# Performance work log

Hardware: AMD Instinct MI355X
Metric: run time of the kernel (lower is better)

Reference implementation:

```python
import jax, jax.numpy as jnp
import numpy as np
import math

D_MODEL = 1024
NUM_HEADS = 16
D_HEAD = D_MODEL // NUM_HEADS
BATCH = 2
SEQ = 2048
ROPE_BASE = 10000.0


def get_rotary_embedding(seq_len, d_head):
    # standard RoPE tables: cos/sin of shape [seq_len, d_head]
    inv_freq = 1.0 / (ROPE_BASE ** (jnp.arange(0, d_head, 2, dtype=jnp.float32) / d_head))
    t = jnp.arange(seq_len, dtype=jnp.float32)
    freqs = jnp.outer(t, inv_freq)                      # [S, d_head/2]
    emb = jnp.concatenate([freqs, freqs], axis=-1)      # [S, d_head]
    return jnp.cos(emb), jnp.sin(emb)


def rotate_half(x):
    x1, x2 = jnp.split(x, 2, axis=-1)
    return jnp.concatenate([-x2, x1], axis=-1)


def apply_rotary_pos_emb(x, cos, sin):
    # x: [B, H, S, Dh]; cos/sin: [S, Dh] broadcast over B, H
    return x * cos[None, None, :, :] + rotate_half(x) * sin[None, None, :, :]


def setup_inputs() -> dict:
    key = jax.random.key(0)
    ks = jax.random.split(key, 9)
    s = 1.0 / math.sqrt(D_MODEL)
    inp = {
        "x":  jax.random.normal(ks[0], (BATCH, SEQ, D_MODEL), dtype=jnp.float32),
        "Wq": jax.random.uniform(ks[1], (D_MODEL, D_MODEL), jnp.float32, -s, s),
        "bq": jnp.zeros((D_MODEL,), jnp.float32),
        "Wk": jax.random.uniform(ks[2], (D_MODEL, D_MODEL), jnp.float32, -s, s),
        "bk": jnp.zeros((D_MODEL,), jnp.float32),
        "Wv": jax.random.uniform(ks[3], (D_MODEL, D_MODEL), jnp.float32, -s, s),
        "bv": jnp.zeros((D_MODEL,), jnp.float32),
        "Wo": jax.random.uniform(ks[4], (D_MODEL, D_MODEL), jnp.float32, -s, s),
        "bo": jnp.zeros((D_MODEL,), jnp.float32),
    }
    return inp


def reference(x, Wq, bq, Wk, bk, Wv, bv, Wo, bo) -> jnp.ndarray:
    B, S, _ = x.shape
    H, Dh = NUM_HEADS, D_HEAD

    def proj(W, b):
        y = jnp.einsum('bsd,ed->bse', x, W) + b          # nn.Linear: x @ W^T + b
        return y.reshape(B, S, H, Dh).transpose(0, 2, 1, 3)  # [B,H,S,Dh]

    Q = proj(Wq, bq)
    K = proj(Wk, bk)
    V = proj(Wv, bv)

    cos, sin = get_rotary_embedding(S, Dh)
    Q = apply_rotary_pos_emb(Q, cos, sin)
    K = apply_rotary_pos_emb(K, cos, sin)

    scores = jnp.einsum('bhqd,bhkd->bhqk', Q, K) / math.sqrt(Dh)  # [B,H,S,S]
    causal = jnp.tril(jnp.ones((S, S), dtype=bool))
    scores = jnp.where(causal[None, None, :, :], scores, -jnp.inf)
    attn = jax.nn.softmax(scores, axis=-1)
    # dropout is identity in eval / p=0
    context = jnp.einsum('bhqk,bhkd->bhqd', attn, V)               # [B,H,S,Dh]
    context = context.transpose(0, 2, 1, 3).reshape(B, S, H * Dh)
    return jnp.einsum('bsd,ed->bse', context, Wo) + bo
```

## Files before the change

### kernel.cpp

```cpp
#include <hip/hip_runtime.h>
#include <hip/hip_bf16.h>
#include <math.h>

typedef __attribute__((ext_vector_type(8))) short short8;
typedef __attribute__((ext_vector_type(8))) __bf16 bf16x8;
typedef __attribute__((ext_vector_type(4))) float f32x4;
typedef __attribute__((ext_vector_type(16))) float f32x16;

#define D_MODEL 1024
#define NUM_HEADS 16
#define D_HEAD 64
#define BATCH 2
#define SEQ 2048
#define BH (BATCH * NUM_HEADS)
#define MTOT (BATCH * SEQ)

__device__ inline f32x4 mfma16(short8 a, short8 b, f32x4 c) {
  return __builtin_amdgcn_mfma_f32_16x16x32_bf16(
      __builtin_bit_cast(bf16x8, a), __builtin_bit_cast(bf16x8, b), c, 0, 0, 0);
}

__device__ inline f32x16 mfma32(short8 a, short8 b, f32x16 c) {
  return __builtin_amdgcn_mfma_f32_32x32x16_bf16(
      __builtin_bit_cast(bf16x8, a), __builtin_bit_cast(bf16x8, b), c, 0, 0, 0);
}

__device__ inline unsigned short f2b(float f) {
  __hip_bfloat16 h = __float2bfloat16(f);
  return __builtin_bit_cast(unsigned short, h);
}

__device__ inline unsigned cvt_pk_bf16(float lo, float hi) {
  unsigned r;
  asm("v_cvt_pk_bf16_f32 %0, %1, %2" : "=v"(r) : "v"(lo), "v"(hi));
  return r;
}

__device__ inline float exp2_hw(float x) {
  float r;
  asm("v_exp_f32 %0, %1" : "=v"(r) : "v"(x));
  return r;
}

__device__ inline void permlane32_swap(unsigned& a, unsigned& b) {
  asm("v_permlane32_swap_b32 %0, %1" : "+v"(a), "+v"(b));
}

__device__ __forceinline__ void wait_barrier_vm0() {
  asm volatile("s_waitcnt vmcnt(0)\n\ts_barrier" ::: "memory");
}

#define GLOAD_LDS16(gaddr, laddr)                                              \
  __builtin_amdgcn_global_load_lds(                                            \
      (const __attribute__((address_space(1))) void*)(gaddr),                  \
      (__attribute__((address_space(3))) void*)(laddr), 16, 0, 0)

__global__ void cvt_f32_bf16(const float* __restrict__ in,
                             unsigned short* __restrict__ out, int n) {
  int i = (blockIdx.x * 256 + threadIdx.x) * 4;
  if (i >= n) return;
  float4 v = *(const float4*)(in + i);
  ushort4 o;
  o.x = f2b(v.x); o.y = f2b(v.y); o.z = f2b(v.z); o.w = f2b(v.w);
  *(ushort4*)(out + i) = o;
}

__global__ void cvt4_f32_bf16(const float* __restrict__ w0, const float* __restrict__ w1,
                              const float* __restrict__ w2, const float* __restrict__ w3,
                              unsigned short* __restrict__ o0, unsigned short* __restrict__ o1,
                              unsigned short* __restrict__ o2, unsigned short* __restrict__ o3,
                              int n) {
  const float* in; unsigned short* out;
  switch (blockIdx.y) {
    case 0: in = w0; out = o0; break;
    case 1: in = w1; out = o1; break;
    case 2: in = w2; out = o2; break;
    default: in = w3; out = o3; break;
  }
  int i = (blockIdx.x * 256 + threadIdx.x) * 4;
  if (i >= n) return;
  float4 v = *(const float4*)(in + i);
  ushort4 o;
  o.x = f2b(v.x); o.y = f2b(v.y); o.z = f2b(v.z); o.w = f2b(v.w);
  *(ushort4*)(out + i) = o;
}

__global__ void trig_kernel(float2* __restrict__ tct) {
  int idx = blockIdx.x * 256 + threadIdx.x;
  int i = idx & 31;
  int s = idx >> 5;
  float inv = powf(10000.0f, -(float)i / 32.0f);
  float t = (float)s * inv;
  tct[idx] = make_float2(cosf(t), sinf(t));
}

#define STAGE64(t, bufi)                                                        \
  do {                                                                          \
    const int _k0 = (t) * 64;                                                   \
    const int _gc = ((lane & 7) ^ (lane >> 3)) * 8;                             \
    const int _lc = (lane & 7) * 8;                                             \
    for (int j = 0; j < 4; j++) {                                               \
      const int _r = w * 32 + j * 8 + (lane >> 3);                              \
      GLOAD_LDS16(&A[(size_t)(bm + _r) * D_MODEL + _k0 + _gc], &As[bufi][_r][_lc]); \
      GLOAD_LDS16(&Bp[(size_t)(bn + _r) * D_MODEL + _k0 + _gc], &Bs[bufi][_r][_lc]); \
    }                                                                           \
  } while (0)

#define KLOOP64()                                                               \
  do {                                                                          \
    const int NT = D_MODEL / 64;                                                \
    STAGE64(0, 0);                                                              \
    for (int t = 0; t < NT; ++t) {                                              \
      const int cur = t & 1;                                                    \
      wait_barrier_vm0();                                                       \
      if (t + 1 < NT) STAGE64(t + 1, cur ^ 1);                                  \
      for (int kk = 0; kk < 2; kk++) {                                          \
        short8 af[4], bf4[4];                                                   \
        for (int mi = 0; mi < 4; mi++)                                          \
          af[mi] = *(const short8*)&As[cur][wr + mi * 16 + fr]                  \
                                         [(kk * 32 + fk) ^ ((fr & 7) << 3)];    \
        for (int ni = 0; ni < 4; ni++)                                          \
          bf4[ni] = *(const short8*)&Bs[cur][wc + ni * 16 + fr]                 \
                                          [(kk * 32 + fk) ^ ((fr & 7) << 3)];   \
        __builtin_amdgcn_s_setprio(1);                                          \
        for (int mi = 0; mi < 4; mi++)                                          \
          for (int ni = 0; ni < 4; ni++)                                        \
            acc[mi][ni] = mfma16(af[mi], bf4[ni], acc[mi][ni]);                 \
        __builtin_amdgcn_s_setprio(0);                                          \
      }                                                                         \
    }                                                                           \
  } while (0)

__global__ __launch_bounds__(256) void gemm_qkv(
    const unsigned short* __restrict__ A,
    const unsigned short* __restrict__ Bp,
    const float* __restrict__ bq, const float* __restrict__ bk,
    const float* __restrict__ bv,
    const float2* __restrict__ tct,
    unsigned short* __restrict__ Qb, unsigned short* __restrict__ Kb,
    unsigned short* __restrict__ Vt) {
  __shared__ unsigned short As[2][128][64];
  __shared__ unsigned short Bs[2][128][64];
  const int bm = blockIdx.y * 128;
  const int bn = blockIdx.x * 128;
  const int tid = threadIdx.x;
  const int lane = tid & 63;
  const int w = tid >> 6;
  const int wr = (w >> 1) * 64, wc = (w & 1) * 64;
  const int fr = lane & 15;
  const int g = lane >> 4;
  const int fk = g * 8;

  f32x4 acc[4][4] = {};
  KLOOP64();

  const int type = bn >> 10;
  const int cloc = (bn & 1023) + wc;
  if (type <= 1) {
    const float* bias = (type == 0) ? bq : bk;
    unsigned short* outp = (type == 0) ? Qb : Kb;
    const float SC = (type == 0) ? 0.125f * 1.44269504f : 1.0f;
    const int h = cloc >> 6;
    for (int mi = 0; mi < 4; mi++)
      for (int r = 0; r < 4; r++) {
        int row = bm + wr + mi * 16 + g * 4 + r;
        int b = row >> 11, s = row & (SEQ - 1);
        size_t base = (((size_t)(b * NUM_HEADS + h)) * SEQ + s) * 64;
        for (int ni = 0; ni < 2; ni++) {
          int i = ni * 16 + fr;
          float x0 = acc[mi][ni][r] + bias[cloc + i];
          float x1 = acc[mi][ni + 2][r] + bias[cloc + i + 32];
          float2 cs = tct[s * 32 + i];
          outp[base + i]      = f2b((x0 * cs.x - x1 * cs.y) * SC);
          outp[base + i + 32] = f2b((x1 * cs.x + x0 * cs.y) * SC);
        }
      }
  } else {
    for (int mi = 0; mi < 4; mi++) {
      int row0 = bm + wr + mi * 16 + g * 4;
      int b = row0 >> 11, s0 = row0 & (SEQ - 1);
      for (int ni = 0; ni < 4; ni++) {
        int col = cloc + ni * 16 + fr;
        int h = col >> 6, dh = col & 63;
        float bvv = bv[col];
        uint2 pk = make_uint2(
            cvt_pk_bf16(acc[mi][ni][0] + bvv, acc[mi][ni][1] + bvv),
            cvt_pk_bf16(acc[mi][ni][2] + bvv, acc[mi][ni][3] + bvv));
        *(uint2*)&Vt[(((size_t)(b * NUM_HEADS + h)) * 64 + dh) * SEQ + s0] = pk;
      }
    }
  }
}

__global__ __launch_bounds__(256) void gemm_out(
    const unsigned short* __restrict__ A,
    const unsigned short* __restrict__ Bp,
    const float* __restrict__ bias,
    float* __restrict__ outf) {
  __shared__ unsigned short As[2][128][64];
  __shared__ unsigned short Bs[2][128][64];
  const int bm = blockIdx.y * 128;
  const int bn = blockIdx.x * 128;
  const int tid = threadIdx.x;
  const int lane = tid & 63;
  const int w = tid >> 6;
  const int wr = (w >> 1) * 64, wc = (w & 1) * 64;
  const int fr = lane & 15;
  const int g = lane >> 4;
  const int fk = g * 8;

  f32x4 acc[4][4] = {};
  KLOOP64();

  for (int mi = 0; mi < 4; mi++)
    for (int ni = 0; ni < 4; ni++)
      for (int r = 0; r < 4; r++) {
        int row = bm + wr + mi * 16 + g * 4 + r;
        int col = bn + wc + ni * 16 + fr;
        outf[(size_t)row * D_MODEL + col] = acc[mi][ni][r] + bias[col];
      }
}

__global__ __launch_bounds__(256) void flash_attn(
    const unsigned short* __restrict__ Q,
    const unsigned short* __restrict__ Km,
    const unsigned short* __restrict__ Vt,
    unsigned short* __restrict__ ctx) {
  __shared__ unsigned short Ks[64 * 64];
  __shared__ unsigned short Vs[64 * 64];
  const int bh = blockIdx.x;
  const int by = blockIdx.y;
  const int qt = (by < 8) ? (15 - by) : (by - 8);
  const int tid = threadIdx.x;
  const int lane = tid & 63;
  const int w = tid >> 6;
  const int q31 = lane & 31;
  const int hi = lane >> 5;

  const unsigned short* Qp = Q + (size_t)bh * SEQ * 64;
  const unsigned short* Kp = Km + (size_t)bh * SEQ * 64;
  const unsigned short* Vp = Vt + (size_t)bh * 64 * SEQ;
  const int b = bh >> 4, h = bh & 15;

  const int qbase = qt * 128;
  const int qrow0 = qbase + w * 32;
  const int wmax = qrow0 + 31;
  const int q = qrow0 + q31;

  short8 qf[4];
  for (int s = 0; s < 4; s++)
    qf[s] = *(const short8*)&Qp[(size_t)q * 64 + s * 16 + hi * 8];

  const int srow = tid >> 2;
  const int ss0 = (tid & 3) * 2, ss1 = ss0 + 1;
  const int lw0 = srow * 64 + ((ss0 ^ (srow & 7)) * 8);
  const int lw1 = srow * 64 + ((ss1 ^ (srow & 7)) * 8);

  short8 krA = *(const short8*)&Kp[(size_t)srow * 64 + ss0 * 8];
  short8 krB = *(const short8*)&Kp[(size_t)srow * 64 + ss1 * 8];
  short8 vrA = *(const short8*)&Vp[(size_t)srow * SEQ + ss0 * 8];
  short8 vrB = *(const short8*)&Vp[(size_t)srow * SEQ + ss1 * 8];

  f32x16 oacc0 = {}, oacc1 = {};
  float lq = 0.f;
  const int NSTEPS = 2 * qt + 2;

  for (int step = 0; step < NSTEPS; ++step) {
    const int kbase = step * 64;
    *(short8*)&Ks[lw0] = krA;
    *(short8*)&Ks[lw1] = krB;
    *(short8*)&Vs[lw0] = vrA;
    *(short8*)&Vs[lw1] = vrB;
    __syncthreads();
    if (step + 1 < NSTEPS) {
      const int nk = kbase + 64;
      krA = *(const short8*)&Kp[(size_t)(nk + srow) * 64 + ss0 * 8];
      krB = *(const short8*)&Kp[(size_t)(nk + srow) * 64 + ss1 * 8];
      vrA = *(const short8*)&Vp[(size_t)srow * SEQ + nk + ss0 * 8];
      vrB = *(const short8*)&Vp[(size_t)srow * SEQ + nk + ss1 * 8];
    }

    if (kbase <= wmax) {
      for (int kt = 0; kt < 2; kt++) {
        const int ktb = kbase + kt * 32;
        if (ktb <= wmax) {
          f32x16 sacc = {};
          const int krow = kt * 32 + q31;
          const int kro = krow * 64;
          const int ksw = krow & 7;
          for (int s = 0; s < 4; s++) {
            short8 kf = *(const short8*)&Ks[kro + (((s * 2 + hi) ^ ksw) * 8)];
            sacc = mfma32(kf, qf[s], sacc);
          }
          const bool maskT = (ktb + 31 > qrow0);
          float p[16];
          float rs = 0.f;
#pragma unroll
          for (int reg = 0; reg < 16; reg++) {
            float sv = sacc[reg];
            if (maskT) {
              int key = ktb + (reg & 3) + 8 * (reg >> 2) + 4 * hi;
              sv = (key <= q) ? sv : -INFINITY;
            }
            p[reg] = exp2_hw(sv);
            rs += p[reg];
          }
          lq += rs;
          short8 paf[2];
#pragma unroll
          for (int sl = 0; sl < 2; sl++) {
            const int o = sl * 8;
            unsigned a0 = cvt_pk_bf16(p[o + 0], p[o + 1]);
            unsigned b0 = cvt_pk_bf16(p[o + 4], p[o + 5]);
            permlane32_swap(a0, b0);
            unsigned a1 = cvt_pk_bf16(p[o + 2], p[o + 3]);
            unsigned b1 = cvt_pk_bf16(p[o + 6], p[o + 7]);
            permlane32_swap(a1, b1);
            uint4 u = make_uint4(a0, a1, b0, b1);
            paf[sl] = __builtin_bit_cast(short8, u);
          }
#pragma unroll
          for (int dt = 0; dt < 2; dt++) {
            const int vrow = dt * 32 + q31;
            const int vro = vrow * 64;
            const int vsw = vrow & 7;
#pragma unroll
            for (int sl = 0; sl < 2; sl++) {
              short8 vf = *(const short8*)&Vs[vro + (((kt * 4 + sl * 2 + hi) ^ vsw) * 8)];
              if (dt == 0) oacc0 = mfma32(paf[sl], vf, oacc0);
              else         oacc1 = mfma32(paf[sl], vf, oacc1);
            }
          }
        }
      }
    }
    __syncthreads();
  }

  lq += __shfl_xor(lq, 32);
#pragma unroll
  for (int reg = 0; reg < 16; reg++) {
    const int crow = (reg & 3) + 8 * (reg >> 2) + 4 * hi;
    const float linv = 1.f / __shfl(lq, crow);
    const int row = qrow0 + crow;
    size_t base = ((size_t)b * SEQ + row) * D_MODEL + h * 64 + q31;
    ctx[base]      = f2b(oacc0[reg] * linv);
    ctx[base + 32] = f2b(oacc1[reg] * linv);
  }
}

extern "C" void kernel_launch(void* const* d_in, const int* in_sizes, int n_in,
                              void* d_out, int out_size, void* d_ws, size_t ws_size,
                              hipStream_t stream) {
  const float* x  = (const float*)d_in[0];
  const float* Wq = (const float*)d_in[1];
  const float* bq = (const float*)d_in[2];
  const float* Wk = (const float*)d_in[3];
  const float* bk = (const float*)d_in[4];
  const float* Wv = (const float*)d_in[5];
  const float* bv = (const float*)d_in[6];
  const float* Wo = (const float*)d_in[7];
  const float* bo = (const float*)d_in[8];
  float* out = (float*)d_out;

  char* ws = (char*)d_ws;
  size_t off = 0;
  auto alloc = [&](size_t bytes) {
    char* p = ws + off;
    off += (bytes + 255) & ~(size_t)255;
    return p;
  };
  unsigned short* xb   = (unsigned short*)alloc((size_t)MTOT * D_MODEL * 2);
  unsigned short* wqkv = (unsigned short*)alloc((size_t)3 * D_MODEL * D_MODEL * 2);
  unsigned short* wob  = (unsigned short*)alloc((size_t)D_MODEL * D_MODEL * 2);
  unsigned short* Qb   = (unsigned short*)alloc((size_t)BH * SEQ * 64 * 2);
  unsigned short* Kb   = (unsigned short*)alloc((size_t)BH * SEQ * 64 * 2);
  unsigned short* Vt   = (unsigned short*)alloc((size_t)BH * 64 * SEQ * 2);
  unsigned short* ctxb = (unsigned short*)alloc((size_t)MTOT * D_MODEL * 2);
  float2* tct = (float2*)alloc((size_t)SEQ * 32 * 8);

  int nx = MTOT * D_MODEL;
  int nw = D_MODEL * D_MODEL;
  cvt_f32_bf16<<<nx / 1024, 256, 0, stream>>>(x, xb, nx);
  cvt4_f32_bf16<<<dim3(nw / 1024, 4), 256, 0, stream>>>(
      Wq, Wk, Wv, Wo, wqkv, wqkv + nw, wqkv + 2 * (size_t)nw, wob, nw);
  trig_kernel<<<SEQ * 32 / 256, 256, 0, stream>>>(tct);

  gemm_qkv<<<dim3(3 * D_MODEL / 128, MTOT / 128), 256, 0, stream>>>(
      xb, wqkv, bq, bk, bv, tct, Qb, Kb, Vt);

  flash_attn<<<dim3(BH, 16), 256, 0, stream>>>(Qb, Kb, Vt, ctxb);

  gemm_out<<<dim3(D_MODEL / 128, MTOT / 128), 256, 0, stream>>>(ctxb, wob, bo, out);
}
```

Measured before the change: 123.9 us.

## Shrink flash attention blocks to 64 query rows with two waves, longest-first order

The flash attention kernel now uses 128-thread blocks covering 64 query rows instead of 256-thread blocks covering 128, doubling the grid to 32 query tiles per head. Tiles are scheduled heaviest-first (descending qb) instead of the previous paired ordering. Each thread now stages four K and four V vectors per step. The smaller blocks cut wasted causal work at the diagonal and give finer load balance. The cost is that each K/V tile loaded into shared memory is reused by half as many query rows.

```diff
diff --git a/kernel.cpp b/kernel.cpp
--- a/kernel.cpp
+++ b/kernel.cpp
@@ -221,7 +221,7 @@
       }
 }
 
-__global__ __launch_bounds__(256) void flash_attn(
+__global__ __launch_bounds__(128) void flash_attn(
     const unsigned short* __restrict__ Q,
     const unsigned short* __restrict__ Km,
     const unsigned short* __restrict__ Vt,
@@ -229,8 +229,7 @@
   __shared__ unsigned short Ks[64 * 64];
   __shared__ unsigned short Vs[64 * 64];
   const int bh = blockIdx.x;
-  const int by = blockIdx.y;
-  const int qt = (by < 8) ? (15 - by) : (by - 8);
+  const int qb = 31 - (int)blockIdx.y;
   const int tid = threadIdx.x;
   const int lane = tid & 63;
   const int w = tid >> 6;
@@ -242,94 +241,96 @@
   const unsigned short* Vp = Vt + (size_t)bh * 64 * SEQ;
   const int b = bh >> 4, h = bh & 15;
 
-  const int qbase = qt * 128;
-  const int qrow0 = qbase + w * 32;
+  const int qrow0 = qb * 64 + w * 32;
   const int wmax = qrow0 + 31;
   const int q = qrow0 + q31;
 
   short8 qf[4];
+#pragma unroll
   for (int s = 0; s < 4; s++)
     qf[s] = *(const short8*)&Qp[(size_t)q * 64 + s * 16 + hi * 8];
 
-  const int srow = tid >> 2;
-  const int ss0 = (tid & 3) * 2, ss1 = ss0 + 1;
-  const int lw0 = srow * 64 + ((ss0 ^ (srow & 7)) * 8);
-  const int lw1 = srow * 64 + ((ss1 ^ (srow & 7)) * 8);
-
-  short8 krA = *(const short8*)&Kp[(size_t)srow * 64 + ss0 * 8];
-  short8 krB = *(const short8*)&Kp[(size_t)srow * 64 + ss1 * 8];
-  short8 vrA = *(const short8*)&Vp[(size_t)srow * SEQ + ss0 * 8];
-  short8 vrB = *(const short8*)&Vp[(size_t)srow * SEQ + ss1 * 8];
+  const int srow = tid >> 1;
+  const int sb = (tid & 1) * 4;
+  short8 kst[4], vst[4];
+#pragma unroll
+  for (int j = 0; j < 4; j++) {
+    kst[j] = *(const short8*)&Kp[(size_t)srow * 64 + (sb + j) * 8];
+    vst[j] = *(const short8*)&Vp[(size_t)srow * SEQ + (sb + j) * 8];
+  }
 
   f32x16 oacc0 = {}, oacc1 = {};
   float lq = 0.f;
-  const int NSTEPS = 2 * qt + 2;
+  const int NSTEPS = qb + 1;
 
   for (int step = 0; step < NSTEPS; ++step) {
     const int kbase = step * 64;
-    *(short8*)&Ks[lw0] = krA;
-    *(short8*)&Ks[lw1] = krB;
-    *(short8*)&Vs[lw0] = vrA;
-    *(short8*)&Vs[lw1] = vrB;
+#pragma unroll
+    for (int j = 0; j < 4; j++) {
+      const int off = srow * 64 + (((sb + j) ^ (srow & 7)) * 8);
+      *(short8*)&Ks[off] = kst[j];
+      *(short8*)&Vs[off] = vst[j];
+    }
     __syncthreads();
     if (step + 1 < NSTEPS) {
       const int nk = kbase + 64;
-      krA = *(const short8*)&Kp[(size_t)(nk + srow) * 64 + ss0 * 8];
-      krB = *(const short8*)&Kp[(size_t)(nk + srow) * 64 + ss1 * 8];
-      vrA = *(const short8*)&Vp[(size_t)srow * SEQ + nk + ss0 * 8];
-      vrB = *(const short8*)&Vp[(size_t)srow * SEQ + nk + ss1 * 8];
+#pragma unroll
+      for (int j = 0; j < 4; j++) {
+        kst[j] = *(const short8*)&Kp[(size_t)(nk + srow) * 64 + (sb + j) * 8];
+        vst[j] = *(const short8*)&Vp[(size_t)srow * SEQ + nk + (sb + j) * 8];
+      }
     }
 
-    if (kbase <= wmax) {
-      for (int kt = 0; kt < 2; kt++) {
-        const int ktb = kbase + kt * 32;
-        if (ktb <= wmax) {
-          f32x16 sacc = {};
-          const int krow = kt * 32 + q31;
-          const int kro = krow * 64;
-          const int ksw = krow & 7;
-          for (int s = 0; s < 4; s++) {
-            short8 kf = *(const short8*)&Ks[kro + (((s * 2 + hi) ^ ksw) * 8)];
-            sacc = mfma32(kf, qf[s], sacc);
+#pragma unroll
+    for (int kt = 0; kt < 2; kt++) {
+      const int ktb = kbase + kt * 32;
+      if (ktb <= wmax) {
+        f32x16 sacc = {};
+        const int krow = kt * 32 + q31;
+        const int kro = krow * 64;
+        const int ksw = krow & 7;
+#pragma unroll
+        for (int s = 0; s < 4; s++) {
+          short8 kf = *(const short8*)&Ks[kro + (((s * 2 + hi) ^ ksw) * 8)];
+          sacc = mfma32(kf, qf[s], sacc);
+        }
+        const bool maskT = (ktb + 31 > qrow0);
+        float p[16];
+        float rs = 0.f;
+#pragma unroll
+        for (int reg = 0; reg < 16; reg++) {
+          float sv = sacc[reg];
+          if (maskT) {
+            int key = ktb + (reg & 3) + 8 * (reg >> 2) + 4 * hi;
+            sv = (key <= q) ? sv : -INFINITY;
           }
-          const bool maskT = (ktb + 31 > qrow0);
-          float p[16];
-          float rs = 0.f;
-#pragma unroll
-          for (int reg = 0; reg < 16; reg++) {
-            float sv = sacc[reg];
-            if (maskT) {
-              int key = ktb + (reg & 3) + 8 * (reg >> 2) + 4 * hi;
-              sv = (key <= q) ? sv : -INFINITY;
-            }
-            p[reg] = exp2_hw(sv);
-            rs += p[reg];
-          }
-          lq += rs;
-          short8 paf[2];
+          p[reg] = exp2_hw(sv);
+          rs += p[reg];
+        }
+        lq += rs;
+        short8 paf[2];
+#pragma unroll
+        for (int sl = 0; sl < 2; sl++) {
+          const int o = sl * 8;
+          unsigned a0 = cvt_pk_bf16(p[o + 0], p[o + 1]);
+          unsigned b0 = cvt_pk_bf16(p[o + 4], p[o + 5]);
+          permlane32_swap(a0, b0);
+          unsigned a1 = cvt_pk_bf16(p[o + 2], p[o + 3]);
+          unsigned b1 = cvt_pk_bf16(p[o + 6], p[o + 7]);
+          permlane32_swap(a1, b1);
+          uint4 u = make_uint4(a0, a1, b0, b1);
+          paf[sl] = __builtin_bit_cast(short8, u);
+        }
+#pragma unroll
+        for (int dt = 0; dt < 2; dt++) {
+          const int vrow = dt * 32 + q31;
+          const int vro = vrow * 64;
+          const int vsw = vrow & 7;
 #pragma unroll
           for (int sl = 0; sl < 2; sl++) {
-            const int o = sl * 8;
-            unsigned a0 = cvt_pk_bf16(p[o + 0], p[o + 1]);
-            unsigned b0 = cvt_pk_bf16(p[o + 4], p[o + 5]);
-            permlane32_swap(a0, b0);
-            unsigned a1 = cvt_pk_bf16(p[o + 2], p[o + 3]);
-            unsigned b1 = cvt_pk_bf16(p[o + 6], p[o + 7]);
-            permlane32_swap(a1, b1);
-            uint4 u = make_uint4(a0, a1, b0, b1);
-            paf[sl] = __builtin_bit_cast(short8, u);
-          }
-#pragma unroll
-          for (int dt = 0; dt < 2; dt++) {
-            const int vrow = dt * 32 + q31;
-            const int vro = vrow * 64;
-            const int vsw = vrow & 7;
-#pragma unroll
-            for (int sl = 0; sl < 2; sl++) {
-              short8 vf = *(const short8*)&Vs[vro + (((kt * 4 + sl * 2 + hi) ^ vsw) * 8)];
-              if (dt == 0) oacc0 = mfma32(paf[sl], vf, oacc0);
-              else         oacc1 = mfma32(paf[sl], vf, oacc1);
-            }
+            short8 vf = *(const short8*)&Vs[vro + (((kt * 4 + sl * 2 + hi) ^ vsw) * 8)];
+            if (dt == 0) oacc0 = mfma32(paf[sl], vf, oacc0);
+            else         oacc1 = mfma32(paf[sl], vf, oacc1);
           }
         }
       }
@@ -389,7 +390,7 @@
   gemm_qkv<<<dim3(3 * D_MODEL / 128, MTOT / 128), 256, 0, stream>>>(
       xb, wqkv, bq, bk, bv, tct, Qb, Kb, Vt);
 
-  flash_attn<<<dim3(BH, 16), 256, 0, stream>>>(Qb, Kb, Vt, ctxb);
+  flash_attn<<<dim3(BH, 32), 128, 0, stream>>>(Qb, Kb, Vt, ctxb);
 
   gemm_out<<<dim3(D_MODEL / 128, MTOT / 128), 256, 0, stream>>>(ctxb, wob, bo, out);
 }
```

After: 127.9 us. 1.03x slower.

## Split long causal query tiles across KV chunks with separate combine kernel

Applied to the files above, without the earlier changes.

Flash attention now splits each query tile's key range into chunks of up to 8 KV steps, so long tiles are spread across up to four blocks (split-K / flash-decoding style). Partial unnormalized outputs and row sums go to fp32 workspace, and a new combine kernel sums them and normalizes. This works without max rescaling because the original kernel already uses a fixed-offset exp. The aim is to balance the causal workload and raise the grid from 512 to 1280 blocks. The cost is extra fp32 partial-output traffic and one more kernel launch.

```diff
diff --git a/kernel.cpp b/kernel.cpp
--- a/kernel.cpp
+++ b/kernel.cpp
@@ -225,12 +225,23 @@
     const unsigned short* __restrict__ Q,
     const unsigned short* __restrict__ Km,
     const unsigned short* __restrict__ Vt,
-    unsigned short* __restrict__ ctx) {
+    unsigned short* __restrict__ ctx,
+    float* __restrict__ Opart,
+    float* __restrict__ Lpart) {
   __shared__ unsigned short Ks[64 * 64];
   __shared__ unsigned short Vs[64 * 64];
-  const int bh = blockIdx.x;
-  const int by = blockIdx.y;
-  const int qt = (by < 8) ? (15 - by) : (by - 8);
+  const int x = blockIdx.x;
+  const int bh = blockIdx.y;
+  int qt, ci;
+  if (x < 4)       { qt = x;                  ci = 0; }
+  else if (x < 12) { qt = 4 + ((x - 4) >> 1); ci = (x - 4) & 1; }
+  else if (x < 24) { qt = 8 + (x - 12) / 3;   ci = (x - 12) % 3; }
+  else             { qt = 12 + ((x - 24) >> 2); ci = (x - 24) & 3; }
+  const int T = 2 * qt + 2;
+  const int step0 = ci * 8;
+  const int stepEnd = min(step0 + 8, T);
+  const bool multi = (qt >= 4);
+
   const int tid = threadIdx.x;
   const int lane = tid & 63;
   const int w = tid >> 6;
@@ -248,6 +259,7 @@
   const int q = qrow0 + q31;
 
   short8 qf[4];
+#pragma unroll
   for (int s = 0; s < 4; s++)
     qf[s] = *(const short8*)&Qp[(size_t)q * 64 + s * 16 + hi * 8];
 
@@ -256,23 +268,23 @@
   const int lw0 = srow * 64 + ((ss0 ^ (srow & 7)) * 8);
   const int lw1 = srow * 64 + ((ss1 ^ (srow & 7)) * 8);
 
-  short8 krA = *(const short8*)&Kp[(size_t)srow * 64 + ss0 * 8];
-  short8 krB = *(const short8*)&Kp[(size_t)srow * 64 + ss1 * 8];
-  short8 vrA = *(const short8*)&Vp[(size_t)srow * SEQ + ss0 * 8];
-  short8 vrB = *(const short8*)&Vp[(size_t)srow * SEQ + ss1 * 8];
+  const int kv0 = step0 * 64;
+  short8 krA = *(const short8*)&Kp[(size_t)(kv0 + srow) * 64 + ss0 * 8];
+  short8 krB = *(const short8*)&Kp[(size_t)(kv0 + srow) * 64 + ss1 * 8];
+  short8 vrA = *(const short8*)&Vp[(size_t)srow * SEQ + kv0 + ss0 * 8];
+  short8 vrB = *(const short8*)&Vp[(size_t)srow * SEQ + kv0 + ss1 * 8];
 
   f32x16 oacc0 = {}, oacc1 = {};
   float lq = 0.f;
-  const int NSTEPS = 2 * qt + 2;
-
-  for (int step = 0; step < NSTEPS; ++step) {
+
+  for (int step = step0; step < stepEnd; ++step) {
     const int kbase = step * 64;
     *(short8*)&Ks[lw0] = krA;
     *(short8*)&Ks[lw1] = krB;
     *(short8*)&Vs[lw0] = vrA;
     *(short8*)&Vs[lw1] = vrB;
     __syncthreads();
-    if (step + 1 < NSTEPS) {
+    if (step + 1 < stepEnd) {
       const int nk = kbase + 64;
       krA = *(const short8*)&Kp[(size_t)(nk + srow) * 64 + ss0 * 8];
       krB = *(const short8*)&Kp[(size_t)(nk + srow) * 64 + ss1 * 8];
@@ -281,6 +293,7 @@
     }
 
     if (kbase <= wmax) {
+#pragma unroll
       for (int kt = 0; kt < 2; kt++) {
         const int ktb = kbase + kt * 32;
         if (ktb <= wmax) {
@@ -288,6 +301,7 @@
           const int krow = kt * 32 + q31;
           const int kro = krow * 64;
           const int ksw = krow & 7;
+#pragma unroll
           for (int s = 0; s < 4; s++) {
             short8 kf = *(const short8*)&Ks[kro + (((s * 2 + hi) ^ ksw) * 8)];
             sacc = mfma32(kf, qf[s], sacc);
@@ -338,14 +352,61 @@
   }
 
   lq += __shfl_xor(lq, 32);
-#pragma unroll
-  for (int reg = 0; reg < 16; reg++) {
-    const int crow = (reg & 3) + 8 * (reg >> 2) + 4 * hi;
-    const float linv = 1.f / __shfl(lq, crow);
-    const int row = qrow0 + crow;
-    size_t base = ((size_t)b * SEQ + row) * D_MODEL + h * 64 + q31;
-    ctx[base]      = f2b(oacc0[reg] * linv);
-    ctx[base + 32] = f2b(oacc1[reg] * linv);
+
+  if (!multi) {
+#pragma unroll
+    for (int reg = 0; reg < 16; reg++) {
+      const int crow = (reg & 3) + 8 * (reg >> 2) + 4 * hi;
+      const float linv = 1.f / __shfl(lq, crow);
+      const int row = qrow0 + crow;
+      size_t base = ((size_t)b * SEQ + row) * D_MODEL + h * 64 + q31;
+      ctx[base]      = f2b(oacc0[reg] * linv);
+      ctx[base + 32] = f2b(oacc1[reg] * linv);
+    }
+  } else {
+    const size_t cbase = (((size_t)bh * 12 + (qt - 4)) * 4 + ci);
+    if (hi == 0) Lpart[cbase * 128 + w * 32 + q31] = lq;
+#pragma unroll
+    for (int reg = 0; reg < 16; reg++) {
+      const int crow = (reg & 3) + 8 * (reg >> 2) + 4 * hi;
+      const int r = w * 32 + crow;
+      float* Op = &Opart[(cbase * 128 + r) * 64 + q31];
+      Op[0]  = oacc0[reg];
+      Op[32] = oacc1[reg];
+    }
+  }
+}
+
+__global__ __launch_bounds__(256) void combine(
+    const float* __restrict__ Opart, const float* __restrict__ Lpart,
+    unsigned short* __restrict__ ctx) {
+  const int qtp = blockIdx.x;
+  const int bh = blockIdx.y;
+  const int qt = qtp + 4;
+  const int nc = (2 * qt + 9) >> 3;
+  const int b = bh >> 4, h = bh & 15;
+  const int t = threadIdx.x;
+  for (int it = 0; it < 4; ++it) {
+    const int e = it * 2048 + t * 8;
+    const int r = e >> 6, dh = e & 63;
+    float acc[8] = {};
+    float ls = 0.f;
+    for (int ci = 0; ci < nc; ++ci) {
+      const size_t base = (((size_t)bh * 12 + qtp) * 4 + ci) * 128 + r;
+      const float* Op = Opart + base * 64 + dh;
+      float4 a = *(const float4*)Op;
+      float4 c = *(const float4*)(Op + 4);
+      acc[0] += a.x; acc[1] += a.y; acc[2] += a.z; acc[3] += a.w;
+      acc[4] += c.x; acc[5] += c.y; acc[6] += c.z; acc[7] += c.w;
+      ls += Lpart[base];
+    }
+    const float inv = 1.f / ls;
+    unsigned short o[8];
+#pragma unroll
+    for (int j = 0; j < 8; j++) o[j] = f2b(acc[j] * inv);
+    const int row = qt * 128 + r;
+    *(short8*)&ctx[((size_t)b * SEQ + row) * D_MODEL + h * 64 + dh] =
+        *(short8*)o;
   }
 }
 
@@ -378,6 +439,8 @@
   unsigned short* Vt   = (unsigned short*)alloc((size_t)BH * 64 * SEQ * 2);
   unsigned short* ctxb = (unsigned short*)alloc((size_t)MTOT * D_MODEL * 2);
   float2* tct = (float2*)alloc((size_t)SEQ * 32 * 8);
+  float* Opart = (float*)alloc((size_t)32 * 12 * 4 * 128 * 64 * 4);
+  float* Lpart = (float*)alloc((size_t)32 * 12 * 4 * 128 * 4);
 
   int nx = MTOT * D_MODEL;
   int nw = D_MODEL * D_MODEL;
@@ -389,7 +452,8 @@
   gemm_qkv<<<dim3(3 * D_MODEL / 128, MTOT / 128), 256, 0, stream>>>(
       xb, wqkv, bq, bk, bv, tct, Qb, Kb, Vt);
 
-  flash_attn<<<dim3(BH, 16), 256, 0, stream>>>(Qb, Kb, Vt, ctxb);
+  flash_attn<<<dim3(40, BH), 256, 0, stream>>>(Qb, Kb, Vt, ctxb, Opart, Lpart);
+  combine<<<dim3(12, BH), 256, 0, stream>>>(Opart, Lpart, ctxb);
 
   gemm_out<<<dim3(D_MODEL / 128, MTOT / 128), 256, 0, stream>>>(ctxb, wob, bo, out);
 }
```

Measured after the change: 130.1 us. 1.05x slower.

## Use 256x256 tiles with 4-stage pipelined loads in QKV GEMM

Applied to the files above, without the earlier changes.

Rewrites the QKV projection GEMM to use 256x256 output tiles with 512 threads (8 waves, each computing 128x64). The K step drops to 32, and LDS is split into a 4-buffer ring filled three stages ahead, with partial vmcnt waits. The goal is more operand reuse per byte loaded and better latency hiding. The grid shrinks to 12x16=192 blocks, which may underfill the 256 CUs, and register pressure from 32 accumulators per lane rises.

```diff
diff --git a/kernel.cpp b/kernel.cpp
--- a/kernel.cpp
+++ b/kernel.cpp
@@ -48,6 +48,12 @@
 
 __device__ __forceinline__ void wait_barrier_vm0() {
   asm volatile("s_waitcnt vmcnt(0)\n\ts_barrier" ::: "memory");
+}
+__device__ __forceinline__ void wait_barrier_vm4() {
+  asm volatile("s_waitcnt vmcnt(4)\n\ts_barrier" ::: "memory");
+}
+__device__ __forceinline__ void wait_barrier_vm8() {
+  asm volatile("s_waitcnt vmcnt(8)\n\ts_barrier" ::: "memory");
 }
 
 #define GLOAD_LDS16(gaddr, laddr)                                              \
@@ -92,6 +98,109 @@
   float inv = powf(10000.0f, -(float)i / 32.0f);
   float t = (float)s * inv;
   tct[idx] = make_float2(cosf(t), sinf(t));
+}
+
+__global__ __launch_bounds__(512) void gemm_qkv(
+    const unsigned short* __restrict__ A,
+    const unsigned short* __restrict__ Bp,
+    const float* __restrict__ bq, const float* __restrict__ bk,
+    const float* __restrict__ bv,
+    const float2* __restrict__ tct,
+    unsigned short* __restrict__ Qb, unsigned short* __restrict__ Kb,
+    unsigned short* __restrict__ Vt) {
+  __shared__ unsigned short As[4][256][32];
+  __shared__ unsigned short Bs[4][256][32];
+  const int bm = blockIdx.y * 256;
+  const int bn = blockIdx.x * 256;
+  const int tid = threadIdx.x;
+  const int lane = tid & 63;
+  const int wid = tid >> 6;
+  const int wr = (wid >> 2) * 128;
+  const int wc = (wid & 3) * 64;
+  const int fr = lane & 15;
+  const int g = lane >> 4;
+  const int fk = g * 8;
+  const int rsw = (fr & 3) << 3;
+
+  int srow0 = tid >> 2,               slc0 = (tid & 3) * 8;
+  int srow1 = (512 + tid) >> 2,       slc1 = ((512 + tid) & 3) * 8;
+  int sgc0 = (((tid & 3) ^ (srow0 & 3)) * 8);
+  int sgc1 = ((((512 + tid) & 3) ^ (srow1 & 3)) * 8);
+
+#define QSTAGE(t, bi)                                                          \
+  do {                                                                         \
+    const int _k0 = (t) * 32;                                                  \
+    GLOAD_LDS16(&A[(size_t)(bm + srow0) * D_MODEL + _k0 + sgc0], &As[bi][srow0][slc0]); \
+    GLOAD_LDS16(&Bp[(size_t)(bn + srow0) * D_MODEL + _k0 + sgc0], &Bs[bi][srow0][slc0]); \
+    GLOAD_LDS16(&A[(size_t)(bm + srow1) * D_MODEL + _k0 + sgc1], &As[bi][srow1][slc1]); \
+    GLOAD_LDS16(&Bp[(size_t)(bn + srow1) * D_MODEL + _k0 + sgc1], &Bs[bi][srow1][slc1]); \
+  } while (0)
+
+  f32x4 acc[8][4] = {};
+  const int NT = D_MODEL / 32;
+
+  QSTAGE(0, 0);
+  QSTAGE(1, 1);
+  QSTAGE(2, 2);
+  for (int t = 0; t < NT; ++t) {
+    if (t + 2 < NT)      wait_barrier_vm8();
+    else if (t + 1 < NT) wait_barrier_vm4();
+    else                 wait_barrier_vm0();
+    if (t + 3 < NT) QSTAGE(t + 3, (t + 3) & 3);
+    const int cur = t & 3;
+    short8 af[8], bf4[4];
+#pragma unroll
+    for (int mi = 0; mi < 8; mi++)
+      af[mi] = *(const short8*)&As[cur][wr + mi * 16 + fr][fk ^ rsw];
+#pragma unroll
+    for (int ni = 0; ni < 4; ni++)
+      bf4[ni] = *(const short8*)&Bs[cur][wc + ni * 16 + fr][fk ^ rsw];
+    __builtin_amdgcn_s_setprio(1);
+#pragma unroll
+    for (int mi = 0; mi < 8; mi++)
+#pragma unroll
+      for (int ni = 0; ni < 4; ni++)
+        acc[mi][ni] = mfma16(af[mi], bf4[ni], acc[mi][ni]);
+    __builtin_amdgcn_s_setprio(0);
+  }
+
+  const int type = bn >> 10;
+  const int cloc = (bn & 1023) + wc;
+  if (type <= 1) {
+    const float* bias = (type == 0) ? bq : bk;
+    unsigned short* outp = (type == 0) ? Qb : Kb;
+    const float SC = (type == 0) ? 0.125f * 1.44269504f : 1.0f;
+    const int h = cloc >> 6;
+    for (int mi = 0; mi < 8; mi++)
+      for (int r = 0; r < 4; r++) {
+        int row = bm + wr + mi * 16 + g * 4 + r;
+        int b = row >> 11, s = row & (SEQ - 1);
+        size_t base = (((size_t)(b * NUM_HEADS + h)) * SEQ + s) * 64;
+        for (int ni = 0; ni < 2; ni++) {
+          int i = ni * 16 + fr;
+          float x0 = acc[mi][ni][r] + bias[cloc + i];
+          float x1 = acc[mi][ni + 2][r] + bias[cloc + i + 32];
+          float2 cs = tct[s * 32 + i];
+          outp[base + i]      = f2b((x0 * cs.x - x1 * cs.y) * SC);
+          outp[base + i + 32] = f2b((x1 * cs.x + x0 * cs.y) * SC);
+        }
+      }
+  } else {
+    for (int mi = 0; mi < 8; mi++) {
+      int row0 = bm + wr + mi * 16 + g * 4;
+      int b = row0 >> 11, s0 = row0 & (SEQ - 1);
+      for (int ni = 0; ni < 4; ni++) {
+        int col = cloc + ni * 16 + fr;
+        int h = col >> 6, dh = col & 63;
+        float bvv = bv[col];
+        uint2 pk = make_uint2(
+            cvt_pk_bf16(acc[mi][ni][0] + bvv, acc[mi][ni][1] + bvv),
+            cvt_pk_bf16(acc[mi][ni][2] + bvv, acc[mi][ni][3] + bvv));
+        *(uint2*)&Vt[(((size_t)(b * NUM_HEADS + h)) * 64 + dh) * SEQ + s0] = pk;
+      }
+    }
+  }
+#undef QSTAGE
 }
 
 #define STAGE64(t, bufi)                                                        \
@@ -131,67 +240,6 @@
     }                                                                           \
   } while (0)
 
-__global__ __launch_bounds__(256) void gemm_qkv(
-    const unsigned short* __restrict__ A,
-    const unsigned short* __restrict__ Bp,
-    const float* __restrict__ bq, const float* __restrict__ bk,
-    const float* __restrict__ bv,
-    const float2* __restrict__ tct,
-    unsigned short* __restrict__ Qb, unsigned short* __restrict__ Kb,
-    unsigned short* __restrict__ Vt) {
-  __shared__ unsigned short As[2][128][64];
-  __shared__ unsigned short Bs[2][128][64];
-  const int bm = blockIdx.y * 128;
-  const int bn = blockIdx.x * 128;
-  const int tid = threadIdx.x;
-  const int lane = tid & 63;
-  const int w = tid >> 6;
-  const int wr = (w >> 1) * 64, wc = (w & 1) * 64;
-  const int fr = lane & 15;
-  const int g = lane >> 4;
-  const int fk = g * 8;
-
-  f32x4 acc[4][4] = {};
-  KLOOP64();
-
-  const int type = bn >> 10;
-  const int cloc = (bn & 1023) + wc;
-  if (type <= 1) {
-    const float* bias = (type == 0) ? bq : bk;
-    unsigned short* outp = (type == 0) ? Qb : Kb;
-    const float SC = (type == 0) ? 0.125f * 1.44269504f : 1.0f;
-    const int h = cloc >> 6;
-    for (int mi = 0; mi < 4; mi++)
-      for (int r = 0; r < 4; r++) {
-        int row = bm + wr + mi * 16 + g * 4 + r;
-        int b = row >> 11, s = row & (SEQ - 1);
-        size_t base = (((size_t)(b * NUM_HEADS + h)) * SEQ + s) * 64;
-        for (int ni = 0; ni < 2; ni++) {
-          int i = ni * 16 + fr;
-          float x0 = acc[mi][ni][r] + bias[cloc + i];
-          float x1 = acc[mi][ni + 2][r] + bias[cloc + i + 32];
-          float2 cs = tct[s * 32 + i];
-          outp[base + i]      = f2b((x0 * cs.x - x1 * cs.y) * SC);
-          outp[base + i + 32] = f2b((x1 * cs.x + x0 * cs.y) * SC);
-        }
-      }
-  } else {
-    for (int mi = 0; mi < 4; mi++) {
-      int row0 = bm + wr + mi * 16 + g * 4;
-      int b = row0 >> 11, s0 = row0 & (SEQ - 1);
-      for (int ni = 0; ni < 4; ni++) {
-        int col = cloc + ni * 16 + fr;
-        int h = col >> 6, dh = col & 63;
-        float bvv = bv[col];
-        uint2 pk = make_uint2(
-            cvt_pk_bf16(acc[mi][ni][0] + bvv, acc[mi][ni][1] + bvv),
-            cvt_pk_bf16(acc[mi][ni][2] + bvv, acc[mi][ni][3] + bvv));
-        *(uint2*)&Vt[(((size_t)(b * NUM_HEADS + h)) * 64 + dh) * SEQ + s0] = pk;
-      }
-    }
-  }
-}
-
 __global__ __launch_bounds__(256) void gemm_out(
     const unsigned short* __restrict__ A,
     const unsigned short* __restrict__ Bp,
@@ -386,7 +434,7 @@
       Wq, Wk, Wv, Wo, wqkv, wqkv + nw, wqkv + 2 * (size_t)nw, wob, nw);
   trig_kernel<<<SEQ * 32 / 256, 256, 0, stream>>>(tct);
 
-  gemm_qkv<<<dim3(3 * D_MODEL / 128, MTOT / 128), 256, 0, stream>>>(
+  gemm_qkv<<<dim3(3 * D_MODEL / 256, MTOT / 256), 512, 0, stream>>>(
       xb, wqkv, bq, bk, bv, tct, Qb, Kb, Vt);
 
   flash_attn<<<dim3(BH, 16), 256, 0, stream>>>(Qb, Kb, Vt, ctxb);
```

Result: slower. 130.0 us (+4.9%).
